# Performance work log

Measured on AMD Instinct MI355X. Metric: run time of the kernel, lower is better.

Reference implementation:

```python
import jax, jax.numpy as jnp
import numpy as np

D_MODEL = 2048
NUM_HEADS = 32
NUM_KV_GROUPS = 8
D_K = D_MODEL // NUM_HEADS  # 64
KV_DIM = D_K * NUM_KV_GROUPS  # 512
B, S = 2, 2048


def setup_inputs() -> dict:
    key = jax.random.key(0)
    ks = jax.random.split(key, 9)
    sd = 1.0 / np.sqrt(D_MODEL).astype(np.float32)
    return {
        "x": jax.random.normal(ks[0], (B, S, D_MODEL), jnp.float32),
        "wq": jax.random.normal(ks[1], (D_MODEL, D_MODEL), jnp.float32) * sd,
        "bq": jnp.zeros((D_MODEL,), jnp.float32),
        "wk": jax.random.normal(ks[2], (D_MODEL, KV_DIM), jnp.float32) * sd,
        "bk": jnp.zeros((KV_DIM,), jnp.float32),
        "wv": jax.random.normal(ks[3], (D_MODEL, KV_DIM), jnp.float32) * sd,
        "bv": jnp.zeros((KV_DIM,), jnp.float32),
        "wo": jax.random.normal(ks[4], (D_MODEL, D_MODEL), jnp.float32) * sd,
        "bo": jnp.zeros((D_MODEL,), jnp.float32),
    }


def reference(x, wq, bq, wk, bk, wv, bv, wo, bo):
    b, s, _ = x.shape
    # projections (torch Linear = x @ W^T + b; weights here stored as (in,out))
    Q = (x @ wq + bq).reshape(b, s, NUM_HEADS, D_K).transpose(0, 2, 1, 3)       # [B,H,S,dk]
    K = (x @ wk + bk).reshape(b, s, NUM_KV_GROUPS, D_K).transpose(0, 2, 1, 3)   # [B,G,S,dk]
    V = (x @ wv + bv).reshape(b, s, NUM_KV_GROUPS, D_K).transpose(0, 2, 1, 3)   # [B,G,S,dk]
    kv_repeat = NUM_HEADS // NUM_KV_GROUPS
    K_rep = jnp.repeat(K, kv_repeat, axis=1)  # [B,H,S,dk]
    V_rep = jnp.repeat(V, kv_repeat, axis=1)  # [B,H,S,dk]
    scale = 1.0 / jnp.sqrt(jnp.asarray(D_K, x.dtype))
    attn_scores = jnp.einsum("bhqd,bhkd->bhqk", Q, K_rep) * scale
    attn_weights = jax.nn.softmax(attn_scores, axis=-1)                          # [B,H,S,S]
    context = jnp.einsum("bhqk,bhkd->bhqd", attn_weights, V_rep)
    context = context.transpose(0, 2, 1, 3).reshape(b, s, D_MODEL)
    return context @ wo + bo
```

## Files before the change

### kernel.cpp

```cpp
#include <hip/hip_runtime.h>
#include <hip/hip_bf16.h>

typedef __bf16 v8bf16 __attribute__((ext_vector_type(8)));
typedef __bf16 bf16x4 __attribute__((ext_vector_type(4)));
typedef float  f32x4  __attribute__((ext_vector_type(4)));

#define D_MODEL 2048
#define S_LEN   2048
#define NHEADS  32
#define NGROUPS 8
#define DK      64
#define NTOK    4096
#define NQKV    3072
#define QSCALE  0.18033688011112042f

__device__ __forceinline__ void lds_load16(const void* g, void* l) {
  __builtin_amdgcn_global_load_lds(
      (__attribute__((address_space(1))) unsigned int*)g,
      (__attribute__((address_space(3))) unsigned int*)l, 16, 0, 0);
}

__device__ __forceinline__ int sw64(int row, int col) {
  return row * 64 + (col ^ ((row & 7) << 3));
}
__device__ __forceinline__ int swp(int row, int col) {
  return row * 32 + (col ^ (((row >> 2) & 3) << 3));
}

__global__ __launch_bounds__(256)
void cvt_f32_bf16(const float* __restrict__ in, __bf16* __restrict__ out, int n) {
  int i = (blockIdx.x * 256 + threadIdx.x) * 4;
  if (i >= n) return;
  float4 v = *(const float4*)(in + i);
  bf16x4 o = { (__bf16)v.x, (__bf16)v.y, (__bf16)v.z, (__bf16)v.w };
  *(bf16x4*)(out + i) = o;
}

__global__ __launch_bounds__(256)
void transpose_cvt(const float* __restrict__ in, __bf16* __restrict__ out, int R, int C) {
  __shared__ float tile[32][33];
  int tx = threadIdx.x, ty = threadIdx.y;
  int c0 = blockIdx.x * 32, r0 = blockIdx.y * 32;
#pragma unroll
  for (int j = 0; j < 4; j++)
    tile[ty + 8 * j][tx] = in[(size_t)(r0 + ty + 8 * j) * C + c0 + tx];
  __syncthreads();
#pragma unroll
  for (int j = 0; j < 4; j++)
    out[(size_t)(c0 + ty + 8 * j) * R + r0 + tx] = (__bf16)tile[tx][ty + 8 * j];
}

__global__ __launch_bounds__(256)
void transpose_bf16(const __bf16* __restrict__ in, __bf16* __restrict__ out,
                    int R, int C, int ldin, int ldout) {
  __shared__ __bf16 tile[32][33];
  int tx = threadIdx.x, ty = threadIdx.y;
  int c0 = blockIdx.x * 32, r0 = blockIdx.y * 32;
#pragma unroll
  for (int j = 0; j < 4; j++)
    tile[ty + 8 * j][tx] = in[(size_t)(r0 + ty + 8 * j) * ldin + c0 + tx];
  __syncthreads();
#pragma unroll
  for (int j = 0; j < 4; j++)
    out[(size_t)(c0 + ty + 8 * j) * ldout + r0 + tx] = tile[tx][ty + 8 * j];
}

template <int MODE>
__global__ __launch_bounds__(256, 2)
void gemm_bt(const __bf16* __restrict__ A, const __bf16* __restrict__ BT,
             const float* __restrict__ b0, const float* __restrict__ b1,
             const float* __restrict__ b2,
             __bf16* __restrict__ Cb, float* __restrict__ Cf,
             int M, int N, int K) {
  __shared__ __bf16 As[128 * 32];
  __shared__ __bf16 Bs[128 * 32];
  const int t = threadIdx.x;
  const int lane = t & 63, w = t >> 6;
  const int lr = lane & 15, lg = lane >> 4;
  const int m0 = blockIdx.y * 128, n0 = blockIdx.x * 128;
  const int rm = (w >> 1) * 64, cn = (w & 1) * 64;
  const int srow = t >> 2, scol = (t & 3) * 8;

  const f32x4 fz = {0.f, 0.f, 0.f, 0.f};
  f32x4 acc[4][4];
#pragma unroll
  for (int mi = 0; mi < 4; mi++)
#pragma unroll
    for (int ni = 0; ni < 4; ni++) acc[mi][ni] = fz;

  for (int kt = 0; kt < K; kt += 32) {
    __syncthreads();
    lds_load16(A + (size_t)(m0 + srow) * K + kt + scol, As + w * 512);
    lds_load16(A + (size_t)(m0 + 64 + srow) * K + kt + scol, As + 2048 + w * 512);
    lds_load16(BT + (size_t)(n0 + srow) * K + kt + scol, Bs + w * 512);
    lds_load16(BT + (size_t)(n0 + 64 + srow) * K + kt + scol, Bs + 2048 + w * 512);
    __syncthreads();
    v8bf16 af[4], bfr[4];
#pragma unroll
    for (int i = 0; i < 4; i++)
      af[i] = *(const v8bf16*)&As[(rm + i * 16 + lr) * 32 + lg * 8];
#pragma unroll
    for (int i = 0; i < 4; i++)
      bfr[i] = *(const v8bf16*)&Bs[(cn + i * 16 + lr) * 32 + lg * 8];
#pragma unroll
    for (int mi = 0; mi < 4; mi++)
#pragma unroll
      for (int ni = 0; ni < 4; ni++)
        acc[mi][ni] = __builtin_amdgcn_mfma_f32_16x16x32_bf16(af[mi], bfr[ni], acc[mi][ni], 0, 0, 0);
  }

#pragma unroll
  for (int ni = 0; ni < 4; ni++) {
    int col = n0 + cn + ni * 16 + lr;
    float bias, scale = 1.0f;
    if (MODE == 0) {
      if (col < 2048)      { bias = b0[col];        scale = QSCALE; }
      else if (col < 2560) { bias = b1[col - 2048]; }
      else                 { bias = b2[col - 2560]; }
    } else {
      bias = b0[col];
    }
#pragma unroll
    for (int mi = 0; mi < 4; mi++)
#pragma unroll
      for (int r = 0; r < 4; r++) {
        int row = m0 + rm + mi * 16 + lg * 4 + r;
        float v = acc[mi][ni][r] + bias;
        if (MODE == 0) Cb[(size_t)row * N + col] = (__bf16)(v * scale);
        else           Cf[(size_t)row * N + col] = v;
      }
  }
}

__global__ __launch_bounds__(256, 4)
void attn_kernel(const __bf16* __restrict__ QKV, const __bf16* __restrict__ VT,
                 __bf16* __restrict__ ctx) {
  __shared__ __bf16 smem[20480];
  const int t = threadIdx.x;
  const int lane = t & 63, w = t >> 6;
  const int lr = lane & 15, lg = lane >> 4;
  const int qt = blockIdx.x, bh = blockIdx.y;
  const int b = bh >> 5, h = bh & 31, g = h >> 2;
  const int q0 = qt * 128;
  const int scol = (((t & 7) ^ ((t >> 3) & 7)) << 3);

  v8bf16 qa[2][2];
#pragma unroll
  for (int mi = 0; mi < 2; mi++)
#pragma unroll
    for (int ks = 0; ks < 2; ks++)
      qa[mi][ks] = *(const v8bf16*)(QKV +
          (size_t)(b * S_LEN + q0 + w * 32 + mi * 16 + lr) * NQKV + h * DK + ks * 32 + lg * 8);

  const __bf16* ksrc0 = QKV + (size_t)(b * S_LEN + (t >> 3)) * NQKV + D_MODEL + g * DK + scol;
  const __bf16* vsrc0 = VT + (size_t)(g * DK + (t >> 3)) * NTOK + b * S_LEN + scol;

  lds_load16(ksrc0, smem + w * 512);
  lds_load16(ksrc0 + (size_t)32 * NQKV, smem + 2048 + w * 512);
  lds_load16(vsrc0, smem + 4096 + w * 512);
  lds_load16(vsrc0 + (size_t)32 * NTOK, smem + 4096 + 2048 + w * 512);
  __syncthreads();

  float lsum[2][4];
  const f32x4 fz = {0.f, 0.f, 0.f, 0.f};
  f32x4 o[2][4];
#pragma unroll
  for (int mi = 0; mi < 2; mi++) {
#pragma unroll
    for (int r = 0; r < 4; r++) lsum[mi][r] = 0.f;
#pragma unroll
    for (int nd = 0; nd < 4; nd++) o[mi][nd] = fz;
  }
  __bf16* Pw = smem + 16384 + w * 1024;
  int cur = 0;

  for (int kt = 0; kt < 32; kt++) {
    if (kt < 31) {
      __bf16* nb = smem + (cur ^ 1) * 8192;
      const __bf16* kn = ksrc0 + (size_t)(kt + 1) * 64 * NQKV;
      const __bf16* vn = vsrc0 + (size_t)(kt + 1) * 64;
      lds_load16(kn, nb + w * 512);
      lds_load16(kn + (size_t)32 * NQKV, nb + 2048 + w * 512);
      lds_load16(vn, nb + 4096 + w * 512);
      lds_load16(vn + (size_t)32 * NTOK, nb + 4096 + 2048 + w * 512);
    }
    const __bf16* Kb = smem + cur * 8192;
    const __bf16* Vb = Kb + 4096;

    f32x4 s[2][4];
#pragma unroll
    for (int mi = 0; mi < 2; mi++)
#pragma unroll
      for (int ni = 0; ni < 4; ni++) s[mi][ni] = fz;
    __builtin_amdgcn_s_setprio(1);
#pragma unroll
    for (int ks = 0; ks < 2; ks++)
#pragma unroll
      for (int ni = 0; ni < 4; ni++) {
        v8bf16 kb = *(const v8bf16*)&Kb[sw64(ni * 16 + lr, ks * 32 + lg * 8)];
#pragma unroll
        for (int mi = 0; mi < 2; mi++)
          s[mi][ni] = __builtin_amdgcn_mfma_f32_16x16x32_bf16(qa[mi][ks], kb, s[mi][ni], 0, 0, 0);
      }
    __builtin_amdgcn_s_setprio(0);

#pragma unroll
    for (int ks = 0; ks < 2; ks++) {
#pragma unroll
      for (int mi = 0; mi < 2; mi++)
#pragma unroll
        for (int r = 0; r < 4; r++) {
#pragma unroll
          for (int ni2 = 0; ni2 < 2; ni2++) {
            float p = exp2f(s[mi][2 * ks + ni2][r]);
            lsum[mi][r] += p;
            Pw[swp(mi * 16 + lg * 4 + r, ni2 * 16 + lr)] = (__bf16)p;
          }
        }
      v8bf16 pa[2];
#pragma unroll
      for (int mi = 0; mi < 2; mi++)
        pa[mi] = *(const v8bf16*)&Pw[swp(mi * 16 + lr, lg * 8)];
      __builtin_amdgcn_s_setprio(1);
#pragma unroll
      for (int nd = 0; nd < 4; nd++) {
        v8bf16 vb = *(const v8bf16*)&Vb[sw64(nd * 16 + lr, ks * 32 + lg * 8)];
#pragma unroll
        for (int mi = 0; mi < 2; mi++)
          o[mi][nd] = __builtin_amdgcn_mfma_f32_16x16x32_bf16(pa[mi], vb, o[mi][nd], 0, 0, 0);
      }
      __builtin_amdgcn_s_setprio(0);
    }

    __syncthreads();
    cur ^= 1;
  }

#pragma unroll
  for (int mi = 0; mi < 2; mi++)
#pragma unroll
    for (int r = 0; r < 4; r++) {
      float l = lsum[mi][r];
      l += __shfl_xor(l, 1, 16);
      l += __shfl_xor(l, 2, 16);
      l += __shfl_xor(l, 4, 16);
      l += __shfl_xor(l, 8, 16);
      float inv = 1.0f / l;
      int row = b * S_LEN + q0 + w * 32 + mi * 16 + lg * 4 + r;
#pragma unroll
      for (int nd = 0; nd < 4; nd++)
        ctx[(size_t)row * D_MODEL + h * DK + nd * 16 + lr] = (__bf16)(o[mi][nd][r] * inv);
    }
}

extern "C" void kernel_launch(void* const* d_in, const int* in_sizes, int n_in,
                              void* d_out, int out_size, void* d_ws, size_t ws_size,
                              hipStream_t stream) {
  (void)in_sizes; (void)n_in; (void)out_size; (void)ws_size;
  const float* x  = (const float*)d_in[0];
  const float* wq = (const float*)d_in[1];
  const float* bq = (const float*)d_in[2];
  const float* wk = (const float*)d_in[3];
  const float* bk = (const float*)d_in[4];
  const float* wv = (const float*)d_in[5];
  const float* bv = (const float*)d_in[6];
  const float* wo = (const float*)d_in[7];
  const float* bo = (const float*)d_in[8];

  char* ws = (char*)d_ws;
  __bf16* xb    = (__bf16*)(ws);
  __bf16* wqkvT = (__bf16*)(ws + 16777216);
  __bf16* woT   = (__bf16*)(ws + 29360128);
  __bf16* QKVb  = (__bf16*)(ws + 37748736);
  __bf16* VbT   = (__bf16*)(ws + 62914560);
  __bf16* ctx   = (__bf16*)(ws + 67108864);

  dim3 tb(32, 8);
  cvt_f32_bf16<<<8192, 256, 0, stream>>>(x, xb, NTOK * D_MODEL);
  transpose_cvt<<<dim3(64, 64), tb, 0, stream>>>(wq, wqkvT, 2048, 2048);
  transpose_cvt<<<dim3(16, 64), tb, 0, stream>>>(wk, wqkvT + 2048 * 2048, 2048, 512);
  transpose_cvt<<<dim3(16, 64), tb, 0, stream>>>(wv, wqkvT + 2560 * 2048, 2048, 512);
  transpose_cvt<<<dim3(64, 64), tb, 0, stream>>>(wo, woT, 2048, 2048);

  gemm_bt<0><<<dim3(24, 32), 256, 0, stream>>>(xb, wqkvT, bq, bk, bv,
                                               QKVb, nullptr, NTOK, NQKV, 2048);
  transpose_bf16<<<dim3(16, 128), tb, 0, stream>>>(QKVb + 2560, VbT, 4096, 512, 3072, 4096);
  attn_kernel<<<dim3(16, 64), 256, 0, stream>>>(QKVb, VbT, ctx);
  gemm_bt<1><<<dim3(16, 32), 256, 0, stream>>>(ctx, woT, bo, nullptr, nullptr,
                                               nullptr, (float*)d_out, NTOK, 2048, 2048);
}
```

Baseline: 249.3 us.

## Transpose QK^T MFMA, compute softmax row sums via ones-MFMA, swizzle block order

The attention kernel now computes S^T by swapping the MFMA operands, so each lane holds four consecutive keys. Those probabilities are packed into one bf16x4 LDS store on a padded P tile instead of scattered scalar stores. The softmax denominator comes from an extra MFMA against a ones vector, which removes the per-element adds and the cross-lane shuffle reduction. Block indices in both the GEMM and the attention kernel are remapped so consecutive workgroups spread across the XCDs, aimed at better L2 reuse. The cost is extra MFMA work for the sums and a smaller LDS footprint with a padded layout.

```diff
diff --git a/kernel.cpp b/kernel.cpp
--- a/kernel.cpp
+++ b/kernel.cpp
@@ -18,13 +18,6 @@
   __builtin_amdgcn_global_load_lds(
       (__attribute__((address_space(1))) unsigned int*)g,
       (__attribute__((address_space(3))) unsigned int*)l, 16, 0, 0);
-}
-
-__device__ __forceinline__ int sw64(int row, int col) {
-  return row * 64 + (col ^ ((row & 7) << 3));
-}
-__device__ __forceinline__ int swp(int row, int col) {
-  return row * 32 + (col ^ (((row >> 2) & 3) << 3));
 }
 
 __global__ __launch_bounds__(256)
@@ -77,7 +70,11 @@
   const int t = threadIdx.x;
   const int lane = t & 63, w = t >> 6;
   const int lr = lane & 15, lg = lane >> 4;
-  const int m0 = blockIdx.y * 128, n0 = blockIdx.x * 128;
+  const int gx = gridDim.x;
+  const int flat = blockIdx.y * gx + blockIdx.x;
+  const int cpx = (gx * gridDim.y) >> 3;
+  const int sb = (flat & 7) * cpx + (flat >> 3);
+  const int m0 = (sb / gx) * 128, n0 = (sb % gx) * 128;
   const int rm = (w >> 1) * 64, cn = (w & 1) * 64;
   const int srow = t >> 2, scol = (t & 3) * 8;
 
@@ -135,11 +132,13 @@
 __global__ __launch_bounds__(256, 4)
 void attn_kernel(const __bf16* __restrict__ QKV, const __bf16* __restrict__ VT,
                  __bf16* __restrict__ ctx) {
-  __shared__ __bf16 smem[20480];
+  __shared__ __bf16 smem[18944];
   const int t = threadIdx.x;
   const int lane = t & 63, w = t >> 6;
   const int lr = lane & 15, lg = lane >> 4;
-  const int qt = blockIdx.x, bh = blockIdx.y;
+  const int flat = blockIdx.y * 16 + blockIdx.x;
+  const int swz = (flat & 7) * 128 + (flat >> 3);
+  const int qt = swz & 15, bh = swz >> 4;
   const int b = bh >> 5, h = bh & 31, g = h >> 2;
   const int q0 = qt * 128;
   const int scol = (((t & 7) ^ ((t >> 3) & 7)) << 3);
@@ -148,9 +147,9 @@
 #pragma unroll
   for (int mi = 0; mi < 2; mi++)
 #pragma unroll
-    for (int ks = 0; ks < 2; ks++)
-      qa[mi][ks] = *(const v8bf16*)(QKV +
-          (size_t)(b * S_LEN + q0 + w * 32 + mi * 16 + lr) * NQKV + h * DK + ks * 32 + lg * 8);
+    for (int dk2 = 0; dk2 < 2; dk2++)
+      qa[mi][dk2] = *(const v8bf16*)(QKV +
+          (size_t)(b * S_LEN + q0 + w * 32 + mi * 16 + lr) * NQKV + h * DK + dk2 * 32 + lg * 8);
 
   const __bf16* ksrc0 = QKV + (size_t)(b * S_LEN + (t >> 3)) * NQKV + D_MODEL + g * DK + scol;
   const __bf16* vsrc0 = VT + (size_t)(g * DK + (t >> 3)) * NTOK + b * S_LEN + scol;
@@ -161,17 +160,19 @@
   lds_load16(vsrc0 + (size_t)32 * NTOK, smem + 4096 + 2048 + w * 512);
   __syncthreads();
 
-  float lsum[2][4];
+  const int kloff0 = lr * 64 + ((lg * 8) ^ ((lr & 7) << 3));
+  const int kloff1 = lr * 64 + ((32 + lg * 8) ^ ((lr & 7) << 3));
+  __bf16* Pw = smem + 16384 + w * 640;
+
+  const __bf16 one1 = (__bf16)1.0f;
+  const v8bf16 ones = { one1, one1, one1, one1, one1, one1, one1, one1 };
   const f32x4 fz = {0.f, 0.f, 0.f, 0.f};
-  f32x4 o[2][4];
-#pragma unroll
-  for (int mi = 0; mi < 2; mi++) {
-#pragma unroll
-    for (int r = 0; r < 4; r++) lsum[mi][r] = 0.f;
+  f32x4 o[2][4], o_sum[2];
+  o_sum[0] = fz; o_sum[1] = fz;
+#pragma unroll
+  for (int mi = 0; mi < 2; mi++)
 #pragma unroll
     for (int nd = 0; nd < 4; nd++) o[mi][nd] = fz;
-  }
-  __bf16* Pw = smem + 16384 + w * 1024;
   int cur = 0;
 
   for (int kt = 0; kt < 32; kt++) {
@@ -185,51 +186,49 @@
       lds_load16(vn + (size_t)32 * NTOK, nb + 4096 + 2048 + w * 512);
     }
     const __bf16* Kb = smem + cur * 8192;
-    const __bf16* Vb = Kb + 4096;
-
-    f32x4 s[2][4];
-#pragma unroll
-    for (int mi = 0; mi < 2; mi++)
-#pragma unroll
-      for (int ni = 0; ni < 4; ni++) s[mi][ni] = fz;
+    const __bf16* k0 = Kb + kloff0;
+    const __bf16* k1 = Kb + kloff1;
+
+    f32x4 st[4][2];
+#pragma unroll
+    for (int ni = 0; ni < 4; ni++) { st[ni][0] = fz; st[ni][1] = fz; }
     __builtin_amdgcn_s_setprio(1);
 #pragma unroll
-    for (int ks = 0; ks < 2; ks++)
-#pragma unroll
-      for (int ni = 0; ni < 4; ni++) {
-        v8bf16 kb = *(const v8bf16*)&Kb[sw64(ni * 16 + lr, ks * 32 + lg * 8)];
-#pragma unroll
-        for (int mi = 0; mi < 2; mi++)
-          s[mi][ni] = __builtin_amdgcn_mfma_f32_16x16x32_bf16(qa[mi][ks], kb, s[mi][ni], 0, 0, 0);
+    for (int ni = 0; ni < 4; ni++) {
+      v8bf16 kb = *(const v8bf16*)(k0 + ni * 1024);
+      st[ni][0] = __builtin_amdgcn_mfma_f32_16x16x32_bf16(kb, qa[0][0], st[ni][0], 0, 0, 0);
+      st[ni][1] = __builtin_amdgcn_mfma_f32_16x16x32_bf16(kb, qa[1][0], st[ni][1], 0, 0, 0);
+    }
+#pragma unroll
+    for (int ni = 0; ni < 4; ni++) {
+      v8bf16 kb = *(const v8bf16*)(k1 + ni * 1024);
+      st[ni][0] = __builtin_amdgcn_mfma_f32_16x16x32_bf16(kb, qa[0][1], st[ni][0], 0, 0, 0);
+      st[ni][1] = __builtin_amdgcn_mfma_f32_16x16x32_bf16(kb, qa[1][1], st[ni][1], 0, 0, 0);
+    }
+    __builtin_amdgcn_s_setprio(0);
+
+#pragma unroll
+    for (int ks = 0; ks < 2; ks++) {
+      const __bf16* vbase = (ks ? k1 : k0) + 4096;
+#pragma unroll
+      for (int mi = 0; mi < 2; mi++) {
+#pragma unroll
+        for (int ni2 = 0; ni2 < 2; ni2++) {
+          f32x4 sv = st[2 * ks + ni2][mi];
+          bf16x4 pk = { (__bf16)exp2f(sv[0]), (__bf16)exp2f(sv[1]),
+                        (__bf16)exp2f(sv[2]), (__bf16)exp2f(sv[3]) };
+          *(bf16x4*)(Pw + lr * 40 + ni2 * 16 + lg * 4) = pk;
+        }
+        v8bf16 pa = *(const v8bf16*)(Pw + lr * 40 + lg * 8);
+        __builtin_amdgcn_s_setprio(1);
+#pragma unroll
+        for (int nd = 0; nd < 4; nd++) {
+          v8bf16 vb = *(const v8bf16*)(vbase + nd * 1024);
+          o[mi][nd] = __builtin_amdgcn_mfma_f32_16x16x32_bf16(pa, vb, o[mi][nd], 0, 0, 0);
+        }
+        o_sum[mi] = __builtin_amdgcn_mfma_f32_16x16x32_bf16(pa, ones, o_sum[mi], 0, 0, 0);
+        __builtin_amdgcn_s_setprio(0);
       }
-    __builtin_amdgcn_s_setprio(0);
-
-#pragma unroll
-    for (int ks = 0; ks < 2; ks++) {
-#pragma unroll
-      for (int mi = 0; mi < 2; mi++)
-#pragma unroll
-        for (int r = 0; r < 4; r++) {
-#pragma unroll
-          for (int ni2 = 0; ni2 < 2; ni2++) {
-            float p = exp2f(s[mi][2 * ks + ni2][r]);
-            lsum[mi][r] += p;
-            Pw[swp(mi * 16 + lg * 4 + r, ni2 * 16 + lr)] = (__bf16)p;
-          }
-        }
-      v8bf16 pa[2];
-#pragma unroll
-      for (int mi = 0; mi < 2; mi++)
-        pa[mi] = *(const v8bf16*)&Pw[swp(mi * 16 + lr, lg * 8)];
-      __builtin_amdgcn_s_setprio(1);
-#pragma unroll
-      for (int nd = 0; nd < 4; nd++) {
-        v8bf16 vb = *(const v8bf16*)&Vb[sw64(nd * 16 + lr, ks * 32 + lg * 8)];
-#pragma unroll
-        for (int mi = 0; mi < 2; mi++)
-          o[mi][nd] = __builtin_amdgcn_mfma_f32_16x16x32_bf16(pa[mi], vb, o[mi][nd], 0, 0, 0);
-      }
-      __builtin_amdgcn_s_setprio(0);
     }
 
     __syncthreads();
@@ -240,12 +239,7 @@
   for (int mi = 0; mi < 2; mi++)
 #pragma unroll
     for (int r = 0; r < 4; r++) {
-      float l = lsum[mi][r];
-      l += __shfl_xor(l, 1, 16);
-      l += __shfl_xor(l, 2, 16);
-      l += __shfl_xor(l, 4, 16);
-      l += __shfl_xor(l, 8, 16);
-      float inv = 1.0f / l;
+      float inv = 1.0f / o_sum[mi][r];
       int row = b * S_LEN + q0 + w * 32 + mi * 16 + lg * 4 + r;
 #pragma unroll
       for (int nd = 0; nd < 4; nd++)
```

Result: faster. 242.0 us (-2.9%).
